# Performance work log

Hardware: AMD Instinct MI355X
Metric: run time of the kernel (lower is better)

## Reference

```python
import jax, jax.numpy as jnp
import numpy as np

B, N, C = 4, 49152, 256
E = 393216
CMID = C // 4
K = 3
EPS = 1e-5


def _cheb_prop(x, row, col, a_norm):
    # L_hat x with lambda_max=2, sym norm: L_hat = -D^{-1/2} A D^{-1/2} (zero diag)
    # x: [B, N, F]
    msg = a_norm[None, :, None] * x[:, col, :]           # [B, E, F]
    return -jnp.zeros_like(x).at[:, row, :].add(msg)


def _cheb_conv(x, row, col, a_norm, W, b):
    # W: [K, Fin, Fout], b: [Fout]
    out = jnp.einsum('bnf,fg->bng', x, W[0])
    Tx0, Tx1 = x, _cheb_prop(x, row, col, a_norm)
    out = out + jnp.einsum('bnf,fg->bng', Tx1, W[1])
    for k in range(2, W.shape[0]):
        Tx2 = 2.0 * _cheb_prop(Tx1, row, col, a_norm) - Tx0
        out = out + jnp.einsum('bnf,fg->bng', Tx2, W[k])
        Tx0, Tx1 = Tx1, Tx2
    return out + b


def _inst_norm(y):
    # InstanceNorm over the node axis (y viewed as [B, C, N]), affine=False
    mean = jnp.mean(y, axis=1, keepdims=True)
    var = jnp.var(y, axis=1, keepdims=True)
    return (y - mean) * jax.lax.rsqrt(var + EPS)


def setup_inputs() -> dict:
    key = jax.random.key(0)
    ks = jax.random.split(key, 8)
    x = jax.random.normal(ks[0], (B, N, C), dtype=jnp.float32)
    edge_index = jax.random.randint(ks[1], (2, E), 0, N, dtype=jnp.int32)
    edge_weight = jax.random.uniform(ks[2], (E,), dtype=jnp.float32)
    s1 = 1.0 / np.sqrt(C)
    s2 = 1.0 / np.sqrt(CMID)
    W1 = jax.random.normal(ks[3], (K, C, CMID), dtype=jnp.float32) * s1
    W2 = jax.random.normal(ks[4], (K, CMID, CMID), dtype=jnp.float32) * s2
    W3 = jax.random.normal(ks[5], (K, CMID, C), dtype=jnp.float32) * s2
    b1 = jnp.zeros((CMID,), dtype=jnp.float32)
    b2 = jnp.zeros((CMID,), dtype=jnp.float32)
    b3 = jnp.zeros((C,), dtype=jnp.float32)
    return {"x": x, "edge_index": edge_index, "edge_weight": edge_weight,
            "W1": W1, "b1": b1, "W2": W2, "b2": b2, "W3": W3, "b3": b3}


def reference(x, edge_index, edge_weight, W1, b1, W2, b2, W3, b3):
    row, col = edge_index[0], edge_index[1]
    deg = jnp.zeros((N,), dtype=x.dtype).at[row].add(edge_weight)
    dinv = jnp.where(deg > 0, jax.lax.rsqrt(jnp.maximum(deg, EPS)), 0.0)
    a_norm = edge_weight * dinv[row] * dinv[col]

    y = _cheb_conv(x, row, col, a_norm, W1, b1)
    y = jax.nn.relu(_inst_norm(y))
    y = _cheb_conv(y, row, col, a_norm, W2, b2)
    y = jax.nn.relu(_inst_norm(y))
    y = _cheb_conv(y, row, col, a_norm, W3, b3)
    y = jax.nn.relu(_inst_norm(y))
    return y + x
```

## Files before the change

kernel.cpp:

```cpp
#include <hip/hip_runtime.h>

#define NNODES 49152
#define NB 4
#define NE 393216
#define MTOT (NB*NNODES)
#define EPS 1e-5f

typedef __attribute__((ext_vector_type(8))) short s8v;
typedef __attribute__((ext_vector_type(4))) float f32x4;

__device__ inline float b2f(ushort u){ union{uint i; float f;} v; v.i = ((uint)u)<<16; return v.f; }
__device__ inline ushort f2b(float f){ union{float f; uint i;} v; v.f=f; uint r = v.i + 0x7fff + ((v.i>>16)&1); return (ushort)(r>>16); }

__global__ __launch_bounds__(256) void k_deg_cnt(const int* __restrict__ row,
    const float* __restrict__ w, float* __restrict__ deg, int* __restrict__ cnt)
{
    int e = blockIdx.x*256 + threadIdx.x;
    if (e >= NE) return;
    int r = row[e];
    atomicAdd(&deg[r], w[e]);
    atomicAdd(&cnt[r], 1);
}

__global__ __launch_bounds__(256) void k_dinv(const float* __restrict__ deg, float* __restrict__ dinv)
{
    int i = blockIdx.x*256 + threadIdx.x;
    if (i >= NNODES) return;
    float d = deg[i];
    dinv[i] = (d > 0.0f) ? rsqrtf(fmaxf(d, EPS)) : 0.0f;
}

__global__ __launch_bounds__(1024) void k_scan(const int* __restrict__ cnt, int* __restrict__ rowptr)
{
    __shared__ int ssum[1024];
    const int CH = NNODES/1024;
    int t = threadIdx.x;
    int base = t*CH;
    int loc[CH];
    int s = 0;
    #pragma unroll
    for (int i = 0; i < CH; ++i) { loc[i] = s; s += cnt[base+i]; }
    ssum[t] = s;
    __syncthreads();
    for (int off = 1; off < 1024; off <<= 1) {
        int v = ssum[t];
        int add = (t >= off) ? ssum[t-off] : 0;
        __syncthreads();
        ssum[t] = v + add;
        __syncthreads();
    }
    int prefix = (t == 0) ? 0 : ssum[t-1];
    #pragma unroll
    for (int i = 0; i < CH; ++i) rowptr[base+i] = prefix + loc[i];
    if (t == 0) rowptr[NNODES] = ssum[1023];
}

__global__ __launch_bounds__(256) void k_fill(const int* __restrict__ row, const int* __restrict__ col,
    const float* __restrict__ w, const float* __restrict__ dinv,
    const int* __restrict__ rowptr, int* __restrict__ fill,
    int* __restrict__ ecol, float* __restrict__ ea)
{
    int e = blockIdx.x*256 + threadIdx.x;
    if (e >= NE) return;
    int r = row[e], c = col[e];
    int pos = rowptr[r] + atomicAdd(&fill[r], 1);
    ecol[pos] = c;
    ea[pos] = w[e] * dinv[r] * dinv[c];
}

__global__ __launch_bounds__(256) void k_packB(const float* __restrict__ W, int Fin, int NF, int K,
    int mode, ushort* __restrict__ out)
{
    int t = blockIdx.x*256 + threadIdx.x;
    int lane = t & 63;
    int fid = t >> 6;
    if (fid >= (K/32)*NF) return;
    int kb = fid / NF, nb = fid % NF;
    int kbase = kb*32 + ((lane>>4)<<3);
    int n0 = nb*16 + (lane&15);
    #pragma unroll
    for (int j = 0; j < 8; ++j) {
        int kk = kbase + j;
        float v;
        if (mode == 0) {
            if (n0 < 64)       v = W[kk*64 + n0] - W[2*Fin*64 + kk*64 + n0];
            else if (n0 < 128) v = W[Fin*64 + kk*64 + (n0-64)];
            else               v = W[2*Fin*64 + kk*64 + (n0-128)];
        } else {
            v = W[(kk>>6)*64*256 + (kk&63)*256 + n0];
        }
        out[((long)fid*64 + lane)*8 + j] = f2b(v);
    }
}

__global__ __launch_bounds__(256,3) void k_gemm1(const float* __restrict__ A,
    const ushort* __restrict__ Bp, ushort* __restrict__ C0, ushort* __restrict__ C1, ushort* __restrict__ C2)
{
    __shared__ ushort Bs[2][6144];
    int tid = threadIdx.x;
    int w = tid >> 6, l = tid & 63;
    int lr = l & 15, kg = l >> 4;
    int n0 = blockIdx.x * 16;

    const float* ap = A + ((long)w*NNODES + n0 + lr)*256 + (kg<<3);
    s8v af[8];
    #pragma unroll
    for (int t = 0; t < 8; ++t) {
        float4 v0 = *(const float4*)(ap + t*32);
        float4 v1 = *(const float4*)(ap + t*32 + 4);
        s8v fr;
        fr[0]=(short)f2b(v0.x); fr[1]=(short)f2b(v0.y); fr[2]=(short)f2b(v0.z); fr[3]=(short)f2b(v0.w);
        fr[4]=(short)f2b(v1.x); fr[5]=(short)f2b(v1.y); fr[6]=(short)f2b(v1.z); fr[7]=(short)f2b(v1.w);
        af[t] = fr;
    }
    f32x4 acc[12];
    #pragma unroll
    for (int nb = 0; nb < 12; ++nb) acc[nb] = (f32x4){0.f,0.f,0.f,0.f};

    #pragma unroll
    for (int ps = 0; ps < 3; ++ps) {
        int off = ps*2048 + tid*8;
        *(s8v*)(&Bs[0][off]) = *(const s8v*)(Bp + off);
    }
    #pragma unroll
    for (int t = 0; t < 8; ++t) {
        __syncthreads();
        s8v stg[3];
        if (t < 7) {
            #pragma unroll
            for (int ps = 0; ps < 3; ++ps)
                stg[ps] = *(const s8v*)(Bp + (long)(t+1)*6144 + ps*2048 + tid*8);
        }
        const ushort* bb = &Bs[t&1][l*8];
        #pragma unroll
        for (int nb = 0; nb < 12; ++nb) {
            s8v bfr = *(const s8v*)(bb + nb*512);
            acc[nb] = __builtin_amdgcn_mfma_f32_16x16x32_bf16(af[t], bfr, acc[nb], 0, 0, 0);
        }
        if (t < 7) {
            #pragma unroll
            for (int ps = 0; ps < 3; ++ps)
                *(s8v*)(&Bs[(t+1)&1][ps*2048 + tid*8]) = stg[ps];
        }
    }
    #pragma unroll
    for (int nb = 0; nb < 12; ++nb) {
        ushort* arr = (nb < 4) ? C0 : ((nb < 8) ? C1 : C2);
        int cc = (nb&3)*16 + lr;
        #pragma unroll
        for (int i = 0; i < 4; ++i) {
            long crow = (long)(n0 + kg*4 + i)*4 + w;
            arr[crow*64 + cc] = f2b(acc[nb][i]);
        }
    }
}

__global__ __launch_bounds__(256,3) void k_gemm2(const ushort* __restrict__ A,
    const ushort* __restrict__ Bp, ushort* __restrict__ C0, ushort* __restrict__ C1, ushort* __restrict__ C2)
{
    __shared__ ushort Bs[12288];
    int tid = threadIdx.x;
    int w = tid >> 6, l = tid & 63;
    int lr = l & 15, kg = l >> 4;
    long rb = (long)blockIdx.x * 64;

    long arow = (rb + w*16 + lr)*64 + (kg<<3);
    s8v af0 = *(const s8v*)(A + arow);
    s8v af1 = *(const s8v*)(A + arow + 32);
    #pragma unroll
    for (int ps = 0; ps < 6; ++ps) {
        int off = ps*2048 + tid*8;
        *(s8v*)(&Bs[off]) = *(const s8v*)(Bp + off);
    }
    f32x4 acc[12];
    #pragma unroll
    for (int nb = 0; nb < 12; ++nb) acc[nb] = (f32x4){0.f,0.f,0.f,0.f};
    __syncthreads();
    #pragma unroll
    for (int t = 0; t < 2; ++t) {
        const ushort* bb = &Bs[t*6144 + l*8];
        s8v afr = t ? af1 : af0;
        #pragma unroll
        for (int nb = 0; nb < 12; ++nb) {
            s8v bfr = *(const s8v*)(bb + nb*512);
            acc[nb] = __builtin_amdgcn_mfma_f32_16x16x32_bf16(afr, bfr, acc[nb], 0, 0, 0);
        }
    }
    #pragma unroll
    for (int nb = 0; nb < 12; ++nb) {
        ushort* arr = (nb < 4) ? C0 : ((nb < 8) ? C1 : C2);
        int cc = (nb&3)*16 + lr;
        #pragma unroll
        for (int i = 0; i < 4; ++i) {
            long crow = rb + w*16 + kg*4 + i;
            arr[crow*64 + cc] = f2b(acc[nb][i]);
        }
    }
}

__global__ __launch_bounds__(256,3) void k_gemm3(const ushort* __restrict__ A0,
    const ushort* __restrict__ A1, const ushort* __restrict__ A2,
    const ushort* __restrict__ Bp, ushort* __restrict__ C, float* __restrict__ Pst)
{
    __shared__ ushort Bs[2][8192];
    int tid = threadIdx.x;
    int w = tid >> 6, l = tid & 63;
    int lr = l & 15, kg = l >> 4;
    long rb = (long)blockIdx.x * 64;

    long arow = (rb + w*16 + lr)*64 + (kg<<3);
    s8v ap[6];
    ap[0] = *(const s8v*)(A0 + arow); ap[1] = *(const s8v*)(A0 + arow + 32);
    ap[2] = *(const s8v*)(A1 + arow); ap[3] = *(const s8v*)(A1 + arow + 32);
    ap[4] = *(const s8v*)(A2 + arow); ap[5] = *(const s8v*)(A2 + arow + 32);
    f32x4 acc[16];
    #pragma unroll
    for (int nb = 0; nb < 16; ++nb) acc[nb] = (f32x4){0.f,0.f,0.f,0.f};

    #pragma unroll
    for (int ps = 0; ps < 4; ++ps) {
        int off = ps*2048 + tid*8;
        *(s8v*)(&Bs[0][off]) = *(const s8v*)(Bp + off);
    }
    #pragma unroll
    for (int t = 0; t < 6; ++t) {
        __syncthreads();
        s8v stg[4];
        if (t < 5) {
            #pragma unroll
            for (int ps = 0; ps < 4; ++ps)
                stg[ps] = *(const s8v*)(Bp + (long)(t+1)*8192 + ps*2048 + tid*8);
        }
        const ushort* bb = &Bs[t&1][l*8];
        #pragma unroll
        for (int nb = 0; nb < 16; ++nb) {
            s8v bfr = *(const s8v*)(bb + nb*512);
            acc[nb] = __builtin_amdgcn_mfma_f32_16x16x32_bf16(ap[t], bfr, acc[nb], 0, 0, 0);
        }
        if (t < 5) {
            #pragma unroll
            for (int ps = 0; ps < 4; ++ps)
                *(s8v*)(&Bs[(t+1)&1][ps*2048 + tid*8]) = stg[ps];
        }
    }
    #pragma unroll
    for (int nb = 0; nb < 16; ++nb) {
        #pragma unroll
        for (int i = 0; i < 4; ++i) {
            long crow = rb + w*16 + kg*4 + i;
            C[crow*256 + nb*16 + lr] = f2b(acc[nb][i]);
        }
    }
    __syncthreads();
    float* Ls = (float*)Bs;
    float* Lq = Ls + 4096;
    #pragma unroll
    for (int nb = 0; nb < 16; ++nb) {
        #pragma unroll
        for (int i = 0; i < 4; ++i) {
            float s = acc[nb][i];
            float q = s*s;
            s += __shfl_xor(s, 16); s += __shfl_xor(s, 32);
            q += __shfl_xor(q, 16); q += __shfl_xor(q, 32);
            if (kg == 0) { Ls[(w*4 + i)*256 + nb*16 + lr] = s; Lq[(w*4 + i)*256 + nb*16 + lr] = q; }
        }
    }
    __syncthreads();
    #pragma unroll
    for (int b = 0; b < 4; ++b) {
        float S = Ls[b*256 + tid] + Ls[(4+b)*256 + tid] + Ls[(8+b)*256 + tid] + Ls[(12+b)*256 + tid];
        float Q = Lq[b*256 + tid] + Lq[(4+b)*256 + tid] + Lq[(8+b)*256 + tid] + Lq[(12+b)*256 + tid];
        Pst[(long)blockIdx.x*2048 + b*256 + tid] = S;
        Pst[(long)blockIdx.x*2048 + 1024 + b*256 + tid] = Q;
    }
}

__global__ __launch_bounds__(256) void k_prop(
    const int* __restrict__ rowptr, const int* __restrict__ ecol, const float* __restrict__ ea,
    const ushort* __restrict__ src, const ushort* __restrict__ basep, float beta,
    ushort* __restrict__ dst, float alpha, float* __restrict__ Pst)
{
    int g = blockIdx.x*8 + (threadIdx.x >> 5);
    int sub = threadIdx.x & 31;
    int e0 = rowptr[g], e1 = rowptr[g+1];
    float acc[8];
    #pragma unroll
    for (int j = 0; j < 8; ++j) acc[j] = 0.f;
    int e = e0;
    for (; e + 4 <= e1; e += 4) {
        int c0 = ecol[e], c1 = ecol[e+1], c2 = ecol[e+2], c3 = ecol[e+3];
        float a0 = ea[e], a1 = ea[e+1], a2 = ea[e+2], a3 = ea[e+3];
        s8v v0 = *(const s8v*)(src + (long)c0*256 + sub*8);
        s8v v1 = *(const s8v*)(src + (long)c1*256 + sub*8);
        s8v v2 = *(const s8v*)(src + (long)c2*256 + sub*8);
        s8v v3 = *(const s8v*)(src + (long)c3*256 + sub*8);
        #pragma unroll
        for (int j = 0; j < 8; ++j)
            acc[j] += a0*b2f((ushort)v0[j]) + a1*b2f((ushort)v1[j])
                    + a2*b2f((ushort)v2[j]) + a3*b2f((ushort)v3[j]);
    }
    for (; e < e1; ++e) {
        int c = ecol[e]; float a = ea[e];
        s8v v = *(const s8v*)(src + (long)c*256 + sub*8);
        #pragma unroll
        for (int j = 0; j < 8; ++j) acc[j] += a*b2f((ushort)v[j]);
    }
    float o[8];
    if (basep) {
        s8v bv = *(const s8v*)(basep + (long)g*256 + sub*8);
        #pragma unroll
        for (int j = 0; j < 8; ++j) o[j] = alpha*acc[j] + beta*b2f((ushort)bv[j]);
    } else {
        #pragma unroll
        for (int j = 0; j < 8; ++j) o[j] = alpha*acc[j];
    }
    s8v ov;
    #pragma unroll
    for (int j = 0; j < 8; ++j) ov[j] = (short)f2b(o[j]);
    *(s8v*)(dst + (long)g*256 + sub*8) = ov;

    if (Pst) {
        __shared__ float Ls[8][256];
        __shared__ float Lq[8][256];
        int grp = threadIdx.x >> 5;
        #pragma unroll
        for (int j = 0; j < 8; ++j) {
            Ls[grp][sub*8 + j] = o[j];
            Lq[grp][sub*8 + j] = o[j]*o[j];
        }
        __syncthreads();
        int t = threadIdx.x;
        float s = 0.f, q = 0.f;
        #pragma unroll
        for (int k = 0; k < 8; ++k) { s += Ls[k][t]; q += Lq[k][t]; }
        Pst[(long)blockIdx.x*512 + t] = s;
        Pst[(long)blockIdx.x*512 + 256 + t] = q;
    }
}

__global__ __launch_bounds__(256) void k_redgen(const float* __restrict__ in, float* __restrict__ out,
    int S, int nin)
{
    int j = blockIdx.x*256 + threadIdx.x;
    int o = blockIdx.y;
    long base = (long)o*nin*S + j;
    float s = 0.f;
    for (int k = 0; k < nin; ++k) s += in[base + (long)k*S];
    out[(long)o*S + j] = s;
}

__global__ __launch_bounds__(256) void k_redfin(const float* __restrict__ in, int S, int nin, int Cw,
    float* __restrict__ mean, float* __restrict__ rs)
{
    int half = S >> 1;
    int j = blockIdx.x*256 + threadIdx.x;
    if (j >= half) return;
    float s = 0.f, q = 0.f;
    for (int k = 0; k < nin; ++k) {
        s += in[(long)k*S + j];
        q += in[(long)k*S + half + j];
    }
    float m = s / (float)NNODES;
    float v = q / (float)NNODES - m*m;
    int b = j / Cw, c = j - b*Cw;
    mean[b*256 + c] = m;
    rs[b*256 + c] = rsqrtf(v + EPS);
}

__global__ __launch_bounds__(256) void k_normrelu(const ushort* __restrict__ y,
    const float* __restrict__ mean, const float* __restrict__ rs, ushort* __restrict__ X)
{
    int t = threadIdx.x;
    long e = (long)blockIdx.x*2048 + t*8;
    int b = (t>>3)&3, c0 = (t&7)*8;
    s8v v = *(const s8v*)(y + e);
    float4 m0 = *(const float4*)(mean + b*256 + c0);
    float4 m1 = *(const float4*)(mean + b*256 + c0 + 4);
    float4 r0 = *(const float4*)(rs + b*256 + c0);
    float4 r1 = *(const float4*)(rs + b*256 + c0 + 4);
    float mm[8] = {m0.x,m0.y,m0.z,m0.w,m1.x,m1.y,m1.z,m1.w};
    float rr[8] = {r0.x,r0.y,r0.z,r0.w,r1.x,r1.y,r1.z,r1.w};
    s8v o;
    #pragma unroll
    for (int j = 0; j < 8; ++j) o[j] = (short)f2b(fmaxf((b2f((ushort)v[j]) - mm[j])*rr[j], 0.f));
    *(s8v*)(X + e) = o;
}

__global__ __launch_bounds__(256) void k_final(const ushort* __restrict__ Ybf,
    const float* __restrict__ x, const float* __restrict__ mean, const float* __restrict__ rs,
    float* __restrict__ out)
{
    int t = threadIdx.x;
    long orow = (long)blockIdx.x*8 + (t>>5);
    int c0 = (t&31)*8;
    int b = (int)(orow / NNODES);
    int n = (int)(orow - (long)b*NNODES);
    s8v v = *(const s8v*)(Ybf + ((long)n*4 + b)*256 + c0);
    float4 m0 = *(const float4*)(mean + b*256 + c0);
    float4 m1 = *(const float4*)(mean + b*256 + c0 + 4);
    float4 r0 = *(const float4*)(rs + b*256 + c0);
    float4 r1 = *(const float4*)(rs + b*256 + c0 + 4);
    float mm[8] = {m0.x,m0.y,m0.z,m0.w,m1.x,m1.y,m1.z,m1.w};
    float rr[8] = {r0.x,r0.y,r0.z,r0.w,r1.x,r1.y,r1.z,r1.w};
    const float* xp = x + orow*256 + c0;
    float* op = out + orow*256 + c0;
    #pragma unroll
    for (int j = 0; j < 8; ++j)
        op[j] = fmaxf((b2f((ushort)v[j]) - mm[j])*rr[j], 0.f) + xp[j];
}

extern "C" void kernel_launch(void* const* d_in, const int* in_sizes, int n_in,
                              void* d_out, int out_size, void* d_ws, size_t ws_size,
                              hipStream_t stream)
{
    const float* x  = (const float*)d_in[0];
    const int*   ei = (const int*)d_in[1];
    const float* ew = (const float*)d_in[2];
    const float* W1 = (const float*)d_in[3];
    const float* W2 = (const float*)d_in[5];
    const float* W3 = (const float*)d_in[7];
    const int* row = ei;
    const int* col = ei + NE;

    char* p = (char*)d_ws;
    size_t used = 0;
    auto alloc = [&](size_t bytes) -> void* {
        void* r = p + used;
        used += (bytes + 1023) & ~(size_t)1023;
        return r;
    };
    float* deg   = (float*)alloc((size_t)3*NNODES*4);
    int*   cnt   = (int*)(deg + NNODES);
    int*   fillc = (int*)(deg + 2*NNODES);
    float* dinv  = (float*)alloc((size_t)NNODES*4);
    int*   rowptr= (int*)alloc((size_t)(NNODES+1)*4);
    int*   ecol  = (int*)alloc((size_t)NE*4);
    float* ea    = (float*)alloc((size_t)NE*4);
    float* mrs   = (float*)alloc((size_t)3*2*1024*4);
    ushort* Bp1  = (ushort*)alloc((size_t)256*192*2);
    ushort* Bp2  = (ushort*)alloc((size_t)64*192*2);
    ushort* Bp3  = (ushort*)alloc((size_t)192*256*2);
    ushort* Za   = (ushort*)alloc((size_t)MTOT*64*2);
    ushort* Zb   = (ushort*)alloc((size_t)MTOT*64*2);
    ushort* Zc   = (ushort*)alloc((size_t)MTOT*64*2);
    ushort* Zd   = (ushort*)alloc((size_t)MTOT*64*2);
    float* Pbig  = (float*)alloc((size_t)6144*512*4);
    float* PPa   = (float*)alloc((size_t)256*2048*4);
    float* PPb   = (float*)alloc((size_t)16*2048*4);
    ushort* Ybf  = (ushort*)alloc((size_t)MTOT*256*2);
    if (ws_size < used) return;

    float* mean1 = mrs;          float* rs1 = mrs + 1024;
    float* mean2 = mrs + 2048;   float* rs2 = mrs + 3072;
    float* mean3 = mrs + 4096;   float* rs3 = mrs + 5120;
    float* Pst3  = (float*)d_out;

    hipMemsetAsync(deg, 0, (size_t)3*NNODES*4, stream);
    k_deg_cnt<<<NE/256, 256, 0, stream>>>(row, ew, deg, cnt);
    k_dinv<<<NNODES/256, 256, 0, stream>>>(deg, dinv);
    k_scan<<<1, 1024, 0, stream>>>(cnt, rowptr);
    k_fill<<<NE/256, 256, 0, stream>>>(row, col, ew, dinv, rowptr, fillc, ecol, ea);
    k_packB<<<24, 256, 0, stream>>>(W1, 256, 12, 256, 0, Bp1);
    k_packB<<<6, 256, 0, stream>>>(W2, 64, 12, 64, 0, Bp2);
    k_packB<<<24, 256, 0, stream>>>(W3, 64, 16, 192, 1, Bp3);

    k_gemm1<<<NNODES/16, 256, 0, stream>>>(x, Bp1, Za, Zb, Zc);
    k_prop<<<NNODES/8, 256, 0, stream>>>(rowptr, ecol, ea, Zc, Zb, 1.f, Zb, -2.f, nullptr);
    k_prop<<<NNODES/8, 256, 0, stream>>>(rowptr, ecol, ea, Zb, Za, 1.f, Za, -1.f, Pbig);
    k_redgen<<<dim3(2,512), 256, 0, stream>>>(Pbig, PPa, 512, 12);
    k_redgen<<<dim3(2,32), 256, 0, stream>>>(PPa, PPb, 512, 16);
    k_redfin<<<1, 256, 0, stream>>>(PPb, 512, 32, 64, mean1, rs1);
    k_normrelu<<<MTOT*64/2048, 256, 0, stream>>>(Za, mean1, rs1, Zc);

    k_gemm2<<<MTOT/64, 256, 0, stream>>>(Zc, Bp2, Za, Zb, Zd);
    k_prop<<<NNODES/8, 256, 0, stream>>>(rowptr, ecol, ea, Zd, Zb, 1.f, Zb, -2.f, nullptr);
    k_prop<<<NNODES/8, 256, 0, stream>>>(rowptr, ecol, ea, Zb, Za, 1.f, Za, -1.f, Pbig);
    k_redgen<<<dim3(2,512), 256, 0, stream>>>(Pbig, PPa, 512, 12);
    k_redgen<<<dim3(2,32), 256, 0, stream>>>(PPa, PPb, 512, 16);
    k_redfin<<<1, 256, 0, stream>>>(PPb, 512, 32, 64, mean2, rs2);
    k_normrelu<<<MTOT*64/2048, 256, 0, stream>>>(Za, mean2, rs2, Zc);

    k_prop<<<NNODES/8, 256, 0, stream>>>(rowptr, ecol, ea, Zc, (const ushort*)nullptr, 0.f, Za, -1.f, nullptr);
    k_prop<<<NNODES/8, 256, 0, stream>>>(rowptr, ecol, ea, Za, Zc, -1.f, Zb, -2.f, nullptr);
    k_gemm3<<<MTOT/64, 256, 0, stream>>>(Zc, Za, Zb, Bp3, Ybf, Pst3);
    k_redgen<<<dim3(8,256), 256, 0, stream>>>(Pst3, PPa, 2048, 12);
    k_redgen<<<dim3(8,16), 256, 0, stream>>>(PPa, PPb, 2048, 16);
    k_redfin<<<4, 256, 0, stream>>>(PPb, 2048, 16, 256, mean3, rs3);
    k_final<<<MTOT/8, 256, 0, stream>>>(Ybf, x, mean3, rs3, (float*)d_out);
}
```

Baseline: 618.9 us.

## Fuse instance-norm+ReLU into consumers, batch prop gathers by 8, collapse reduction passes

Removes the standalone normrelu kernels and applies the normalize+ReLU on load inside gemm2, gemm3 and a templated prop kernel. Prop now loads 8 neighbour rows per iteration with clamped padding to raise memory-level parallelism. The two-stage partial-stat reductions are merged into a single wider redgen pass. This saves two full-tensor read/write passes and several launches, at the cost of recomputing the normalization per gathered neighbour in prop (extra ALU) and some wasted padded loads.

```diff
diff --git a/kernel.cpp b/kernel.cpp
--- a/kernel.cpp
+++ b/kernel.cpp
@@ -156,6 +156,7 @@
 }
 
 __global__ __launch_bounds__(256,3) void k_gemm2(const ushort* __restrict__ A,
+    const float* __restrict__ nmean, const float* __restrict__ nrs,
     const ushort* __restrict__ Bp, ushort* __restrict__ C0, ushort* __restrict__ C1, ushort* __restrict__ C2)
 {
     __shared__ ushort Bs[12288];
@@ -165,13 +166,23 @@
     long rb = (long)blockIdx.x * 64;
 
     long arow = (rb + w*16 + lr)*64 + (kg<<3);
-    s8v af0 = *(const s8v*)(A + arow);
-    s8v af1 = *(const s8v*)(A + arow + 32);
+    s8v raw0 = *(const s8v*)(A + arow);
+    s8v raw1 = *(const s8v*)(A + arow + 32);
     #pragma unroll
     for (int ps = 0; ps < 6; ++ps) {
         int off = ps*2048 + tid*8;
         *(s8v*)(&Bs[off]) = *(const s8v*)(Bp + off);
     }
+    int b = lr & 3;
+    s8v af0, af1;
+    #pragma unroll
+    for (int j = 0; j < 8; ++j) {
+        int c0 = (kg<<3) + j, c1 = 32 + (kg<<3) + j;
+        float f0 = fmaxf((b2f((ushort)raw0[j]) - nmean[b*256 + c0]) * nrs[b*256 + c0], 0.f);
+        float f1 = fmaxf((b2f((ushort)raw1[j]) - nmean[b*256 + c1]) * nrs[b*256 + c1], 0.f);
+        af0[j] = (short)f2b(f0);
+        af1[j] = (short)f2b(f1);
+    }
     f32x4 acc[12];
     #pragma unroll
     for (int nb = 0; nb < 12; ++nb) acc[nb] = (f32x4){0.f,0.f,0.f,0.f};
@@ -200,6 +211,7 @@
 
 __global__ __launch_bounds__(256,3) void k_gemm3(const ushort* __restrict__ A0,
     const ushort* __restrict__ A1, const ushort* __restrict__ A2,
+    const float* __restrict__ nmean, const float* __restrict__ nrs,
     const ushort* __restrict__ Bp, ushort* __restrict__ C, float* __restrict__ Pst)
 {
     __shared__ ushort Bs[2][8192];
@@ -210,7 +222,19 @@
 
     long arow = (rb + w*16 + lr)*64 + (kg<<3);
     s8v ap[6];
-    ap[0] = *(const s8v*)(A0 + arow); ap[1] = *(const s8v*)(A0 + arow + 32);
+    {
+        s8v raw0 = *(const s8v*)(A0 + arow);
+        s8v raw1 = *(const s8v*)(A0 + arow + 32);
+        int b = lr & 3;
+        #pragma unroll
+        for (int j = 0; j < 8; ++j) {
+            int c0 = (kg<<3) + j, c1 = 32 + (kg<<3) + j;
+            float f0 = fmaxf((b2f((ushort)raw0[j]) - nmean[b*256 + c0]) * nrs[b*256 + c0], 0.f);
+            float f1 = fmaxf((b2f((ushort)raw1[j]) - nmean[b*256 + c1]) * nrs[b*256 + c1], 0.f);
+            ap[0][j] = (short)f2b(f0);
+            ap[1][j] = (short)f2b(f1);
+        }
+    }
     ap[2] = *(const s8v*)(A1 + arow); ap[3] = *(const s8v*)(A1 + arow + 32);
     ap[4] = *(const s8v*)(A2 + arow); ap[5] = *(const s8v*)(A2 + arow + 32);
     f32x4 acc[16];
@@ -275,41 +299,60 @@
     }
 }
 
+template<int MODE>
 __global__ __launch_bounds__(256) void k_prop(
     const int* __restrict__ rowptr, const int* __restrict__ ecol, const float* __restrict__ ea,
     const ushort* __restrict__ src, const ushort* __restrict__ basep, float beta,
-    ushort* __restrict__ dst, float alpha, float* __restrict__ Pst)
+    ushort* __restrict__ dst, float alpha, float* __restrict__ Pst,
+    const float* __restrict__ nmean, const float* __restrict__ nrs)
 {
     int g = blockIdx.x*8 + (threadIdx.x >> 5);
     int sub = threadIdx.x & 31;
     int e0 = rowptr[g], e1 = rowptr[g+1];
+    float m8[8], r8[8];
+    if (MODE) {
+        #pragma unroll
+        for (int j = 0; j < 8; ++j) {
+            int idx = sub*8 + j;
+            m8[j] = nmean[(idx>>6)*256 + (idx&63)];
+            r8[j] = nrs[(idx>>6)*256 + (idx&63)];
+        }
+    }
     float acc[8];
     #pragma unroll
     for (int j = 0; j < 8; ++j) acc[j] = 0.f;
-    int e = e0;
-    for (; e + 4 <= e1; e += 4) {
-        int c0 = ecol[e], c1 = ecol[e+1], c2 = ecol[e+2], c3 = ecol[e+3];
-        float a0 = ea[e], a1 = ea[e+1], a2 = ea[e+2], a3 = ea[e+3];
-        s8v v0 = *(const s8v*)(src + (long)c0*256 + sub*8);
-        s8v v1 = *(const s8v*)(src + (long)c1*256 + sub*8);
-        s8v v2 = *(const s8v*)(src + (long)c2*256 + sub*8);
-        s8v v3 = *(const s8v*)(src + (long)c3*256 + sub*8);
-        #pragma unroll
-        for (int j = 0; j < 8; ++j)
-            acc[j] += a0*b2f((ushort)v0[j]) + a1*b2f((ushort)v1[j])
-                    + a2*b2f((ushort)v2[j]) + a3*b2f((ushort)v3[j]);
-    }
-    for (; e < e1; ++e) {
-        int c = ecol[e]; float a = ea[e];
-        s8v v = *(const s8v*)(src + (long)c*256 + sub*8);
-        #pragma unroll
-        for (int j = 0; j < 8; ++j) acc[j] += a*b2f((ushort)v[j]);
+    for (int eb = e0; eb < e1; eb += 8) {
+        int cs[8]; float as[8];
+        #pragma unroll
+        for (int k = 0; k < 8; ++k) {
+            int ee = eb + k;
+            int eec = (ee < e1) ? ee : (e1 - 1);
+            cs[k] = ecol[eec];
+            as[k] = (ee < e1) ? ea[eec] : 0.f;
+        }
+        s8v vs[8];
+        #pragma unroll
+        for (int k = 0; k < 8; ++k)
+            vs[k] = *(const s8v*)(src + (long)cs[k]*256 + sub*8);
+        #pragma unroll
+        for (int k = 0; k < 8; ++k) {
+            #pragma unroll
+            for (int j = 0; j < 8; ++j) {
+                float f = b2f((ushort)vs[k][j]);
+                if (MODE == 1) f = fmaxf((f - m8[j])*r8[j], 0.f);
+                acc[j] += as[k]*f;
+            }
+        }
     }
     float o[8];
     if (basep) {
         s8v bv = *(const s8v*)(basep + (long)g*256 + sub*8);
         #pragma unroll
-        for (int j = 0; j < 8; ++j) o[j] = alpha*acc[j] + beta*b2f((ushort)bv[j]);
+        for (int j = 0; j < 8; ++j) {
+            float bf = b2f((ushort)bv[j]);
+            if (MODE == 2) bf = fmaxf((bf - m8[j])*r8[j], 0.f);
+            o[j] = alpha*acc[j] + beta*bf;
+        }
     } else {
         #pragma unroll
         for (int j = 0; j < 8; ++j) o[j] = alpha*acc[j];
@@ -365,25 +408,6 @@
     int b = j / Cw, c = j - b*Cw;
     mean[b*256 + c] = m;
     rs[b*256 + c] = rsqrtf(v + EPS);
-}
-
-__global__ __launch_bounds__(256) void k_normrelu(const ushort* __restrict__ y,
-    const float* __restrict__ mean, const float* __restrict__ rs, ushort* __restrict__ X)
-{
-    int t = threadIdx.x;
-    long e = (long)blockIdx.x*2048 + t*8;
-    int b = (t>>3)&3, c0 = (t&7)*8;
-    s8v v = *(const s8v*)(y + e);
-    float4 m0 = *(const float4*)(mean + b*256 + c0);
-    float4 m1 = *(const float4*)(mean + b*256 + c0 + 4);
-    float4 r0 = *(const float4*)(rs + b*256 + c0);
-    float4 r1 = *(const float4*)(rs + b*256 + c0 + 4);
-    float mm[8] = {m0.x,m0.y,m0.z,m0.w,m1.x,m1.y,m1.z,m1.w};
-    float rr[8] = {r0.x,r0.y,r0.z,r0.w,r1.x,r1.y,r1.z,r1.w};
-    s8v o;
-    #pragma unroll
-    for (int j = 0; j < 8; ++j) o[j] = (short)f2b(fmaxf((b2f((ushort)v[j]) - mm[j])*rr[j], 0.f));
-    *(s8v*)(X + e) = o;
 }
 
 __global__ __launch_bounds__(256) void k_final(const ushort* __restrict__ Ybf,
@@ -445,8 +469,7 @@
     ushort* Zc   = (ushort*)alloc((size_t)MTOT*64*2);
     ushort* Zd   = (ushort*)alloc((size_t)MTOT*64*2);
     float* Pbig  = (float*)alloc((size_t)6144*512*4);
-    float* PPa   = (float*)alloc((size_t)256*2048*4);
-    float* PPb   = (float*)alloc((size_t)16*2048*4);
+    float* PPa   = (float*)alloc((size_t)48*2048*4);
     ushort* Ybf  = (ushort*)alloc((size_t)MTOT*256*2);
     if (ws_size < used) return;
 
@@ -465,26 +488,21 @@
     k_packB<<<24, 256, 0, stream>>>(W3, 64, 16, 192, 1, Bp3);
 
     k_gemm1<<<NNODES/16, 256, 0, stream>>>(x, Bp1, Za, Zb, Zc);
-    k_prop<<<NNODES/8, 256, 0, stream>>>(rowptr, ecol, ea, Zc, Zb, 1.f, Zb, -2.f, nullptr);
-    k_prop<<<NNODES/8, 256, 0, stream>>>(rowptr, ecol, ea, Zb, Za, 1.f, Za, -1.f, Pbig);
-    k_redgen<<<dim3(2,512), 256, 0, stream>>>(Pbig, PPa, 512, 12);
-    k_redgen<<<dim3(2,32), 256, 0, stream>>>(PPa, PPb, 512, 16);
-    k_redfin<<<1, 256, 0, stream>>>(PPb, 512, 32, 64, mean1, rs1);
-    k_normrelu<<<MTOT*64/2048, 256, 0, stream>>>(Za, mean1, rs1, Zc);
-
-    k_gemm2<<<MTOT/64, 256, 0, stream>>>(Zc, Bp2, Za, Zb, Zd);
-    k_prop<<<NNODES/8, 256, 0, stream>>>(rowptr, ecol, ea, Zd, Zb, 1.f, Zb, -2.f, nullptr);
-    k_prop<<<NNODES/8, 256, 0, stream>>>(rowptr, ecol, ea, Zb, Za, 1.f, Za, -1.f, Pbig);
-    k_redgen<<<dim3(2,512), 256, 0, stream>>>(Pbig, PPa, 512, 12);
-    k_redgen<<<dim3(2,32), 256, 0, stream>>>(PPa, PPb, 512, 16);
-    k_redfin<<<1, 256, 0, stream>>>(PPb, 512, 32, 64, mean2, rs2);
-    k_normrelu<<<MTOT*64/2048, 256, 0, stream>>>(Za, mean2, rs2, Zc);
-
-    k_prop<<<NNODES/8, 256, 0, stream>>>(rowptr, ecol, ea, Zc, (const ushort*)nullptr, 0.f, Za, -1.f, nullptr);
-    k_prop<<<NNODES/8, 256, 0, stream>>>(rowptr, ecol, ea, Za, Zc, -1.f, Zb, -2.f, nullptr);
-    k_gemm3<<<MTOT/64, 256, 0, stream>>>(Zc, Za, Zb, Bp3, Ybf, Pst3);
-    k_redgen<<<dim3(8,256), 256, 0, stream>>>(Pst3, PPa, 2048, 12);
-    k_redgen<<<dim3(8,16), 256, 0, stream>>>(PPa, PPb, 2048, 16);
-    k_redfin<<<4, 256, 0, stream>>>(PPb, 2048, 16, 256, mean3, rs3);
+    k_prop<0><<<NNODES/8, 256, 0, stream>>>(rowptr, ecol, ea, Zc, Zb, 1.f, Zb, -2.f, nullptr, nullptr, nullptr);
+    k_prop<0><<<NNODES/8, 256, 0, stream>>>(rowptr, ecol, ea, Zb, Za, 1.f, Za, -1.f, Pbig, nullptr, nullptr);
+    k_redgen<<<dim3(2,48), 256, 0, stream>>>(Pbig, PPa, 512, 128);
+    k_redfin<<<1, 256, 0, stream>>>(PPa, 512, 48, 64, mean1, rs1);
+
+    k_gemm2<<<MTOT/64, 256, 0, stream>>>(Za, mean1, rs1, Bp2, Zb, Zc, Zd);
+    k_prop<0><<<NNODES/8, 256, 0, stream>>>(rowptr, ecol, ea, Zd, Zc, 1.f, Zc, -2.f, nullptr, nullptr, nullptr);
+    k_prop<0><<<NNODES/8, 256, 0, stream>>>(rowptr, ecol, ea, Zc, Zb, 1.f, Zb, -1.f, Pbig, nullptr, nullptr);
+    k_redgen<<<dim3(2,48), 256, 0, stream>>>(Pbig, PPa, 512, 128);
+    k_redfin<<<1, 256, 0, stream>>>(PPa, 512, 48, 64, mean2, rs2);
+
+    k_prop<1><<<NNODES/8, 256, 0, stream>>>(rowptr, ecol, ea, Zb, (const ushort*)nullptr, 0.f, Za, -1.f, nullptr, mean2, rs2);
+    k_prop<2><<<NNODES/8, 256, 0, stream>>>(rowptr, ecol, ea, Za, Zb, -1.f, Zc, -2.f, nullptr, mean2, rs2);
+    k_gemm3<<<MTOT/64, 256, 0, stream>>>(Zb, Za, Zc, mean2, rs2, Bp3, Ybf, Pst3);
+    k_redgen<<<dim3(8,48), 256, 0, stream>>>(Pst3, PPa, 2048, 64);
+    k_redfin<<<4, 256, 0, stream>>>(PPa, 2048, 48, 256, mean3, rs3);
     k_final<<<MTOT/8, 256, 0, stream>>>(Ybf, x, mean3, rs3, (float*)d_out);
 }
```

Measured after the change: 679.5 us. +9.8%, slower.

## Fuse dinv into fill, fold first norm-relu into gemm2, single-pass reductions

Applied to the files above, without the earlier changes.

Removes the k_dinv kernel and computes inverse-sqrt degrees inside k_fill. The first instance-norm plus ReLU is applied to the A operand inside k_gemm2, which drops one k_normrelu pass over the intermediate. The two-stage partial reductions are collapsed into one redgen with larger chunks feeding redfin, and buffer roles are reassigned. Together these cut kernel launches and global traffic, at the cost of less parallelism in the reductions and extra per-element work and scalar loads in gemm2.

```diff
diff --git a/kernel.cpp b/kernel.cpp
--- a/kernel.cpp
+++ b/kernel.cpp
@@ -20,14 +20,6 @@
     int r = row[e];
     atomicAdd(&deg[r], w[e]);
     atomicAdd(&cnt[r], 1);
-}
-
-__global__ __launch_bounds__(256) void k_dinv(const float* __restrict__ deg, float* __restrict__ dinv)
-{
-    int i = blockIdx.x*256 + threadIdx.x;
-    if (i >= NNODES) return;
-    float d = deg[i];
-    dinv[i] = (d > 0.0f) ? rsqrtf(fmaxf(d, EPS)) : 0.0f;
 }
 
 __global__ __launch_bounds__(1024) void k_scan(const int* __restrict__ cnt, int* __restrict__ rowptr)
@@ -56,16 +48,19 @@
 }
 
 __global__ __launch_bounds__(256) void k_fill(const int* __restrict__ row, const int* __restrict__ col,
-    const float* __restrict__ w, const float* __restrict__ dinv,
+    const float* __restrict__ w, const float* __restrict__ deg,
     const int* __restrict__ rowptr, int* __restrict__ fill,
     int* __restrict__ ecol, float* __restrict__ ea)
 {
     int e = blockIdx.x*256 + threadIdx.x;
     if (e >= NE) return;
     int r = row[e], c = col[e];
+    float dr = deg[r], dc = deg[c];
+    float ir = (dr > 0.0f) ? rsqrtf(fmaxf(dr, EPS)) : 0.0f;
+    float ic = (dc > 0.0f) ? rsqrtf(fmaxf(dc, EPS)) : 0.0f;
     int pos = rowptr[r] + atomicAdd(&fill[r], 1);
     ecol[pos] = c;
-    ea[pos] = w[e] * dinv[r] * dinv[c];
+    ea[pos] = w[e] * ir * ic;
 }
 
 __global__ __launch_bounds__(256) void k_packB(const float* __restrict__ W, int Fin, int NF, int K,
@@ -156,6 +151,7 @@
 }
 
 __global__ __launch_bounds__(256,3) void k_gemm2(const ushort* __restrict__ A,
+    const float* __restrict__ nmean, const float* __restrict__ nrs,
     const ushort* __restrict__ Bp, ushort* __restrict__ C0, ushort* __restrict__ C1, ushort* __restrict__ C2)
 {
     __shared__ ushort Bs[12288];
@@ -165,12 +161,22 @@
     long rb = (long)blockIdx.x * 64;
 
     long arow = (rb + w*16 + lr)*64 + (kg<<3);
-    s8v af0 = *(const s8v*)(A + arow);
-    s8v af1 = *(const s8v*)(A + arow + 32);
+    s8v raw0 = *(const s8v*)(A + arow);
+    s8v raw1 = *(const s8v*)(A + arow + 32);
     #pragma unroll
     for (int ps = 0; ps < 6; ++ps) {
         int off = ps*2048 + tid*8;
         *(s8v*)(&Bs[off]) = *(const s8v*)(Bp + off);
+    }
+    int b = lr & 3;
+    s8v af0, af1;
+    #pragma unroll
+    for (int j = 0; j < 8; ++j) {
+        int c0 = (kg<<3) + j, c1 = 32 + (kg<<3) + j;
+        float f0 = fmaxf((b2f((ushort)raw0[j]) - nmean[b*256 + c0]) * nrs[b*256 + c0], 0.f);
+        float f1 = fmaxf((b2f((ushort)raw1[j]) - nmean[b*256 + c1]) * nrs[b*256 + c1], 0.f);
+        af0[j] = (short)f2b(f0);
+        af1[j] = (short)f2b(f1);
     }
     f32x4 acc[12];
     #pragma unroll
@@ -432,7 +438,6 @@
     float* deg   = (float*)alloc((size_t)3*NNODES*4);
     int*   cnt   = (int*)(deg + NNODES);
     int*   fillc = (int*)(deg + 2*NNODES);
-    float* dinv  = (float*)alloc((size_t)NNODES*4);
     int*   rowptr= (int*)alloc((size_t)(NNODES+1)*4);
     int*   ecol  = (int*)alloc((size_t)NE*4);
     float* ea    = (float*)alloc((size_t)NE*4);
@@ -445,8 +450,7 @@
     ushort* Zc   = (ushort*)alloc((size_t)MTOT*64*2);
     ushort* Zd   = (ushort*)alloc((size_t)MTOT*64*2);
     float* Pbig  = (float*)alloc((size_t)6144*512*4);
-    float* PPa   = (float*)alloc((size_t)256*2048*4);
-    float* PPb   = (float*)alloc((size_t)16*2048*4);
+    float* PPa   = (float*)alloc((size_t)48*2048*4);
     ushort* Ybf  = (ushort*)alloc((size_t)MTOT*256*2);
     if (ws_size < used) return;
 
@@ -457,9 +461,8 @@
 
     hipMemsetAsync(deg, 0, (size_t)3*NNODES*4, stream);
     k_deg_cnt<<<NE/256, 256, 0, stream>>>(row, ew, deg, cnt);
-    k_dinv<<<NNODES/256, 256, 0, stream>>>(deg, dinv);
     k_scan<<<1, 1024, 0, stream>>>(cnt, rowptr);
-    k_fill<<<NE/256, 256, 0, stream>>>(row, col, ew, dinv, rowptr, fillc, ecol, ea);
+    k_fill<<<NE/256, 256, 0, stream>>>(row, col, ew, deg, rowptr, fillc, ecol, ea);
     k_packB<<<24, 256, 0, stream>>>(W1, 256, 12, 256, 0, Bp1);
     k_packB<<<6, 256, 0, stream>>>(W2, 64, 12, 64, 0, Bp2);
     k_packB<<<24, 256, 0, stream>>>(W3, 64, 16, 192, 1, Bp3);
@@ -467,24 +470,20 @@
     k_gemm1<<<NNODES/16, 256, 0, stream>>>(x, Bp1, Za, Zb, Zc);
     k_prop<<<NNODES/8, 256, 0, stream>>>(rowptr, ecol, ea, Zc, Zb, 1.f, Zb, -2.f, nullptr);
     k_prop<<<NNODES/8, 256, 0, stream>>>(rowptr, ecol, ea, Zb, Za, 1.f, Za, -1.f, Pbig);
-    k_redgen<<<dim3(2,512), 256, 0, stream>>>(Pbig, PPa, 512, 12);
-    k_redgen<<<dim3(2,32), 256, 0, stream>>>(PPa, PPb, 512, 16);
-    k_redfin<<<1, 256, 0, stream>>>(PPb, 512, 32, 64, mean1, rs1);
-    k_normrelu<<<MTOT*64/2048, 256, 0, stream>>>(Za, mean1, rs1, Zc);
-
-    k_gemm2<<<MTOT/64, 256, 0, stream>>>(Zc, Bp2, Za, Zb, Zd);
-    k_prop<<<NNODES/8, 256, 0, stream>>>(rowptr, ecol, ea, Zd, Zb, 1.f, Zb, -2.f, nullptr);
-    k_prop<<<NNODES/8, 256, 0, stream>>>(rowptr, ecol, ea, Zb, Za, 1.f, Za, -1.f, Pbig);
-    k_redgen<<<dim3(2,512), 256, 0, stream>>>(Pbig, PPa, 512, 12);
-    k_redgen<<<dim3(2,32), 256, 0, stream>>>(PPa, PPb, 512, 16);
-    k_redfin<<<1, 256, 0, stream>>>(PPb, 512, 32, 64, mean2, rs2);
-    k_normrelu<<<MTOT*64/2048, 256, 0, stream>>>(Za, mean2, rs2, Zc);
-
-    k_prop<<<NNODES/8, 256, 0, stream>>>(rowptr, ecol, ea, Zc, (const ushort*)nullptr, 0.f, Za, -1.f, nullptr);
-    k_prop<<<NNODES/8, 256, 0, stream>>>(rowptr, ecol, ea, Za, Zc, -1.f, Zb, -2.f, nullptr);
-    k_gemm3<<<MTOT/64, 256, 0, stream>>>(Zc, Za, Zb, Bp3, Ybf, Pst3);
-    k_redgen<<<dim3(8,256), 256, 0, stream>>>(Pst3, PPa, 2048, 12);
-    k_redgen<<<dim3(8,16), 256, 0, stream>>>(PPa, PPb, 2048, 16);
-    k_redfin<<<4, 256, 0, stream>>>(PPb, 2048, 16, 256, mean3, rs3);
+    k_redgen<<<dim3(2,48), 256, 0, stream>>>(Pbig, PPa, 512, 128);
+    k_redfin<<<1, 256, 0, stream>>>(PPa, 512, 48, 64, mean1, rs1);
+
+    k_gemm2<<<MTOT/64, 256, 0, stream>>>(Za, mean1, rs1, Bp2, Zb, Zc, Zd);
+    k_prop<<<NNODES/8, 256, 0, stream>>>(rowptr, ecol, ea, Zd, Zc, 1.f, Zc, -2.f, nullptr);
+    k_prop<<<NNODES/8, 256, 0, stream>>>(rowptr, ecol, ea, Zc, Zb, 1.f, Zb, -1.f, Pbig);
+    k_redgen<<<dim3(2,48), 256, 0, stream>>>(Pbig, PPa, 512, 128);
+    k_redfin<<<1, 256, 0, stream>>>(PPa, 512, 48, 64, mean2, rs2);
+    k_normrelu<<<MTOT*64/2048, 256, 0, stream>>>(Zb, mean2, rs2, Za);
+
+    k_prop<<<NNODES/8, 256, 0, stream>>>(rowptr, ecol, ea, Za, (const ushort*)nullptr, 0.f, Zb, -1.f, nullptr);
+    k_prop<<<NNODES/8, 256, 0, stream>>>(rowptr, ecol, ea, Zb, Za, -1.f, Zc, -2.f, nullptr);
+    k_gemm3<<<MTOT/64, 256, 0, stream>>>(Za, Zb, Zc, Bp3, Ybf, Pst3);
+    k_redgen<<<dim3(8,48), 256, 0, stream>>>(Pst3, PPa, 2048, 64);
+    k_redfin<<<4, 256, 0, stream>>>(PPa, 2048, 48, 256, mean3, rs3);
     k_final<<<MTOT/8, 256, 0, stream>>>(Ybf, x, mean3, rs3, (float*)d_out);
 }
```

Result: slower. 680.7 us (+10.0%).
